# Kernel optimization log

Hardware: AMD Instinct MI355X
Metric: run time of the kernel (lower is better)

## Reference

```python
import jax, jax.numpy as jnp
from jax import lax
import numpy as np

FEAT_STRIDE = 16
PRE_NMS_TOP_N = 2000
POST_NMS_TOP_N = 300
NMS_THRESH = 0.7


def _whctrs(a):
    w = a[2] - a[0] + 1.0
    h = a[3] - a[1] + 1.0
    return w, h, a[0] + 0.5 * (w - 1.0), a[1] + 0.5 * (h - 1.0)


def _mkanchors(ws, hs, x_ctr, y_ctr):
    ws = np.asarray(ws, dtype=np.float64)
    hs = np.asarray(hs, dtype=np.float64)
    return np.stack([x_ctr - 0.5 * (ws - 1.0), y_ctr - 0.5 * (hs - 1.0),
                     x_ctr + 0.5 * (ws - 1.0), y_ctr + 0.5 * (hs - 1.0)], axis=1)


def generate_anchors(base_size=16, ratios=np.array([0.5, 1.0, 2.0]), scales=np.array([8.0, 16.0, 32.0])):
    base = np.array([1.0, 1.0, float(base_size), float(base_size)]) - 1.0
    w, h, xc, yc = _whctrs(base)
    size = w * h
    ws = np.round(np.sqrt(size / ratios))
    hs = np.round(ws * ratios)
    ratio_anchors = _mkanchors(ws, hs, xc, yc)
    out = []
    for i in range(ratio_anchors.shape[0]):
        w_i, h_i, xc_i, yc_i = _whctrs(ratio_anchors[i])
        out.append(_mkanchors(w_i * scales, h_i * scales, xc_i, yc_i))
    return np.vstack(out).astype(np.float32)


ANCHORS = generate_anchors()  # [A=9, 4]
NUM_ANCHORS = ANCHORS.shape[0]


def _nms_keep(boxes, thresh):
    # boxes [N,4], already sorted by descending score; torchvision IoU convention.
    x1, y1, x2, y2 = boxes[:, 0], boxes[:, 1], boxes[:, 2], boxes[:, 3]
    areas = (x2 - x1) * (y2 - y1)
    xx1 = jnp.maximum(x1[:, None], x1[None, :])
    yy1 = jnp.maximum(y1[:, None], y1[None, :])
    xx2 = jnp.minimum(x2[:, None], x2[None, :])
    yy2 = jnp.minimum(y2[:, None], y2[None, :])
    inter = jnp.clip(xx2 - xx1, 0.0) * jnp.clip(yy2 - yy1, 0.0)
    iou = inter / (areas[:, None] + areas[None, :] - inter + 1e-9)
    n = boxes.shape[0]
    # sup[i, j] True => box i (higher score) suppresses later box j
    sup = (iou > thresh) & jnp.triu(jnp.ones((n, n), bool), 1)

    def body(i, keep):
        return keep & ~(keep[i] & sup[i])

    return lax.fori_loop(0, n, body, jnp.ones((n,), bool))


def setup_inputs() -> dict:
    key = jax.random.key(0)
    k1, k2 = jax.random.split(key)
    B, A, H, W = 8, NUM_ANCHORS, 128, 128
    scores = jax.random.normal(k1, (B, 2 * A, H, W), jnp.float32)
    bbox_deltas = jax.random.normal(k2, (B, 4 * A, H, W), jnp.float32) * 0.2
    im_h = float(H * FEAT_STRIDE)
    im_w = float(W * FEAT_STRIDE)
    im_info = jnp.tile(jnp.array([[im_h, im_w, 1.0]], jnp.float32), (B, 1))
    return {"scores": scores, "bbox_deltas": bbox_deltas, "im_info": im_info}


def reference(scores, bbox_deltas, im_info):
    B, _, H, W = scores.shape
    A = NUM_ANCHORS
    # --- anchor generation over the feature grid ---
    sx = jnp.arange(W, dtype=jnp.float32) * FEAT_STRIDE
    sy = jnp.arange(H, dtype=jnp.float32) * FEAT_STRIDE
    gx, gy = jnp.meshgrid(sx, sy)  # 'xy' indexing matches np.meshgrid default
    shifts = jnp.stack([gx.ravel(), gy.ravel(), gx.ravel(), gy.ravel()], axis=1)  # [K,4]
    anchors = (jnp.asarray(ANCHORS)[None, :, :] + shifts[:, None, :]).reshape(-1, 4)  # [K*A,4]

    obj_scores = scores[:, A:].transpose(0, 2, 3, 1).reshape(B, -1)   # [B, K*A]
    deltas = bbox_deltas.transpose(0, 2, 3, 1).reshape(B, -1, 4)      # [B, K*A, 4]

    # --- bbox_transform_inv ---
    widths = anchors[:, 2] - anchors[:, 0] + 1.0
    heights = anchors[:, 3] - anchors[:, 1] + 1.0
    ctr_x = anchors[:, 0] + 0.5 * widths
    ctr_y = anchors[:, 1] + 0.5 * heights
    dx, dy, dw, dh = deltas[..., 0], deltas[..., 1], deltas[..., 2], deltas[..., 3]
    pred_ctr_x = dx * widths + ctr_x
    pred_ctr_y = dy * heights + ctr_y
    pred_w = jnp.exp(dw) * widths
    pred_h = jnp.exp(dh) * heights
    proposals = jnp.stack([pred_ctr_x - 0.5 * pred_w, pred_ctr_y - 0.5 * pred_h,
                           pred_ctr_x + 0.5 * pred_w, pred_ctr_y + 0.5 * pred_h], axis=-1)

    # --- clip_boxes: im_info[b] = (h, w, scale) ---
    max_x = (im_info[:, 1] - 1.0)[:, None]
    max_y = (im_info[:, 0] - 1.0)[:, None]
    proposals = jnp.stack([
        jnp.clip(proposals[..., 0], 0.0, max_x),
        jnp.clip(proposals[..., 1], 0.0, max_y),
        jnp.clip(proposals[..., 2], 0.0, max_x),
        jnp.clip(proposals[..., 3], 0.0, max_y)], axis=-1)

    # --- pre-NMS top-k by score ---
    _, order = lax.top_k(obj_scores, PRE_NMS_TOP_N)                  # [B, pre]
    top_props = jnp.take_along_axis(proposals, order[..., None], axis=1)  # [B, pre, 4]

    # --- per-image greedy NMS (fixed-size, jit-compatible) ---
    keep = jax.vmap(lambda b: _nms_keep(b, NMS_THRESH))(top_props)   # [B, pre] bool
    sel = jnp.argsort(jnp.where(keep, 0, 1), axis=1, stable=True)[:, :POST_NMS_TOP_N]
    valid = jnp.take_along_axis(keep, sel, axis=1)                   # [B, post]
    out_boxes = jnp.take_along_axis(top_props, sel[..., None], axis=1) * valid[..., None].astype(top_props.dtype)

    batch_idx = jnp.broadcast_to(
        jnp.arange(B, dtype=out_boxes.dtype)[:, None, None], (B, POST_NMS_TOP_N, 1))
    return jnp.concatenate([batch_idx, out_boxes], axis=-1)  # [B, post_nms_topN, 5]
```

## Files before the change

kernel.cpp:

```cpp
#include <hip/hip_runtime.h>

#define NB 8
#define NA 9
#define HH 128
#define WW 128
#define NCELL (HH * WW)
#define NTOT (NCELL * NA)
#define PRE_K 2000
#define POST_K 300
#define CAP 4096
#define HBLK 9
#define NMS_TH 0.7f

__constant__ float c_aw[NA] = {184.f, 368.f, 736.f, 128.f, 256.f, 512.f, 88.f, 176.f, 352.f};
__constant__ float c_ah[NA] = {96.f, 192.f, 384.f, 128.f, 256.f, 512.f, 176.f, 352.f, 704.f};

__device__ __forceinline__ unsigned int sortable(float s) {
    unsigned int u = __float_as_uint(s);
    return (u & 0x80000000u) ? ~u : (u | 0x80000000u);
}

__device__ __forceinline__ unsigned long long shflx64(unsigned long long v, int m) {
    return __shfl_xor(v, m, 64);
}

__global__ __launch_bounds__(1024) void hist0_kernel(const float* __restrict__ scores,
                                                     unsigned int* __restrict__ h0out) {
    __shared__ unsigned int h[2048];
    int b = blockIdx.y, tid = threadIdx.x;
    h[tid] = 0; h[tid + 1024] = 0;
    __syncthreads();
    const float4* sp4 = (const float4*)(scores + (size_t)b * 18 * NCELL + (size_t)NA * NCELL);
    int base4 = blockIdx.x * 4096;
#pragma unroll
    for (int e = 0; e < 4; ++e) {
        float4 v = sp4[base4 + e * 1024 + tid];
        atomicAdd(&h[sortable(v.x) >> 21], 1u);
        atomicAdd(&h[sortable(v.y) >> 21], 1u);
        atomicAdd(&h[sortable(v.z) >> 21], 1u);
        atomicAdd(&h[sortable(v.w) >> 21], 1u);
    }
    __syncthreads();
    unsigned int* o = h0out + ((size_t)(b * HBLK + blockIdx.x)) * 2048;
    o[tid] = h[tid];
    o[tid + 1024] = h[tid + 1024];
}

__global__ __launch_bounds__(1024) void select0_kernel(const unsigned int* __restrict__ h0out,
                                                       uint2* __restrict__ state0,
                                                       unsigned int* __restrict__ gh1,
                                                       int* __restrict__ cnt) {
    __shared__ unsigned int thr[1024];
    int b = blockIdx.x, tid = threadIdx.x;
    if (tid < 128) gh1[b * 128 + tid] = 0;
    if (tid == 0) cnt[b] = 0;
    unsigned int c0 = 0, c1 = 0;
    for (int p = 0; p < HBLK; ++p) {
        const unsigned int* hp = h0out + ((size_t)(b * HBLK + p)) * 2048;
        uint2 v = *(const uint2*)&hp[2 * tid];
        c0 += v.x; c1 += v.y;
    }
    thr[tid] = c0 + c1;
    __syncthreads();
    for (int off = 1; off < 1024; off <<= 1) {
        unsigned int v = (tid + off < 1024) ? thr[tid + off] : 0u;
        __syncthreads();
        thr[tid] += v;
        __syncthreads();
    }
    unsigned int above = (tid < 1023) ? thr[tid + 1] : 0u;
    if (thr[tid] >= (unsigned)PRE_K && above < (unsigned)PRE_K) {
        if (above + c1 >= (unsigned)PRE_K)
            state0[b] = make_uint2((unsigned)(2 * tid + 1), (unsigned)(PRE_K)-above);
        else
            state0[b] = make_uint2((unsigned)(2 * tid), (unsigned)(PRE_K)-above - c1);
    }
}

__global__ __launch_bounds__(1024) void hist1_kernel(const float* __restrict__ scores,
                                                     const uint2* __restrict__ state0,
                                                     unsigned int* __restrict__ gh1) {
    __shared__ unsigned int h[128];
    int b = blockIdx.y, tid = threadIdx.x;
    if (tid < 128) h[tid] = 0;
    __syncthreads();
    unsigned int piv = state0[b].x;
    const float4* sp4 = (const float4*)(scores + (size_t)b * 18 * NCELL + (size_t)NA * NCELL);
    int base4 = blockIdx.x * 4096;
#pragma unroll
    for (int e = 0; e < 4; ++e) {
        float4 v = sp4[base4 + e * 1024 + tid];
        unsigned int u;
        u = sortable(v.x); if ((u >> 21) == piv) atomicAdd(&h[(u >> 14) & 127u], 1u);
        u = sortable(v.y); if ((u >> 21) == piv) atomicAdd(&h[(u >> 14) & 127u], 1u);
        u = sortable(v.z); if ((u >> 21) == piv) atomicAdd(&h[(u >> 14) & 127u], 1u);
        u = sortable(v.w); if ((u >> 21) == piv) atomicAdd(&h[(u >> 14) & 127u], 1u);
    }
    __syncthreads();
    if (tid < 128 && h[tid]) atomicAdd(&gh1[b * 128 + tid], h[tid]);
}

__global__ void select1_kernel(const unsigned int* __restrict__ gh1,
                               const uint2* __restrict__ state0,
                               unsigned int* __restrict__ state1) {
    int b = blockIdx.x, lane = threadIdx.x;
    unsigned int c0 = 0, c1 = 0;
    if (lane < 64) {
        c0 = gh1[b * 128 + 2 * lane];
        c1 = gh1[b * 128 + 2 * lane + 1];
    }
    unsigned int sum = c0 + c1;
#pragma unroll
    for (int off = 1; off < 64; off <<= 1) {
        unsigned int v = __shfl_down(sum, off, 64);
        if (lane + off < 64) sum += v;
    }
    unsigned int above = __shfl_down(sum, 1, 64);
    if (lane == 63) above = 0;
    unsigned int need0 = state0[b].y;
    if (sum >= need0 && above < need0) {
        unsigned int d = (above + c1 >= need0) ? (unsigned)(2 * lane + 1) : (unsigned)(2 * lane);
        unsigned int prefix = (state0[b].x << 7) | d;
        state1[b] = prefix << 14;
    }
}

__global__ void gather_kernel(const float* __restrict__ scores,
                              const unsigned int* __restrict__ state1,
                              int* __restrict__ cnt,
                              unsigned long long* __restrict__ buf) {
    __shared__ unsigned long long lbuf[2048];
    __shared__ int lcnt;
    __shared__ int gbase;
    int b = blockIdx.y;
    int tid = threadIdx.x;
    if (tid == 0) lcnt = 0;
    __syncthreads();
    unsigned int P = state1[b];
    const float4* sp4 = (const float4*)(scores + (size_t)b * 18 * NCELL + (size_t)NA * NCELL);
    int base4 = blockIdx.x * 512;
#pragma unroll
    for (int e = 0; e < 2; ++e) {
        int t4 = base4 + e * 256 + tid;
        float4 v = sp4[t4];
        float el[4] = {v.x, v.y, v.z, v.w};
#pragma unroll
        for (int j = 0; j < 4; ++j) {
            unsigned int u = sortable(el[j]);
            if (u >= P) {
                int idx4 = t4 * 4 + j;
                int a = idx4 >> 14;
                int cell = idx4 & 16383;
                unsigned int i = (unsigned int)cell * 9u + (unsigned int)a;
                int pos = atomicAdd(&lcnt, 1);
                lbuf[pos] = ((unsigned long long)u << 32) |
                            (unsigned long long)(0xFFFFFFFFu - i);
            }
        }
    }
    __syncthreads();
    if (tid == 0) gbase = atomicAdd(&cnt[b], lcnt);
    __syncthreads();
    int m = lcnt, gb = gbase;
    for (int t = tid; t < m; t += 256) {
        int g = gb + t;
        if (g < CAP) buf[(size_t)b * CAP + g] = lbuf[t];
    }
}

#define SHFL_STEP(J)                                                          \
    {                                                                         \
        int d_ = (J) >> 1;                                                    \
        bool keepMax = (((tid & d_) == 0) == (((2u * (unsigned)tid) & k) == 0)); \
        unsigned long long pa = shflx64(va, d_);                              \
        unsigned long long pb = shflx64(vb, d_);                              \
        va = keepMax ? (va > pa ? va : pa) : (va < pa ? va : pa);             \
        vb = keepMax ? (vb > pb ? vb : pb) : (vb < pb ? vb : pb);             \
    }
#define LOCAL_STEP()                                                          \
    {                                                                         \
        bool desc = (((2u * (unsigned)tid) & k) == 0);                        \
        unsigned long long lo = va < vb ? va : vb;                            \
        unsigned long long hi = va < vb ? vb : va;                            \
        va = desc ? hi : lo; vb = desc ? lo : hi;                             \
    }

__global__ __launch_bounds__(1024) void sort_kernel(const unsigned long long* __restrict__ buf,
                                                    const int* __restrict__ cnt,
                                                    unsigned int* __restrict__ topidx) {
    __shared__ unsigned long long s[CAP];
    int b = blockIdx.x;
    int tid = threadIdx.x;
    int n = min(cnt[b], CAP);
    const unsigned long long* src = buf + (size_t)b * CAP;
    if (n <= 2048) {
        unsigned long long va = (2 * tid < n) ? src[2 * tid] : 0ULL;
        unsigned long long vb = (2 * tid + 1 < n) ? src[2 * tid + 1] : 0ULL;
#pragma unroll
        for (unsigned k = 2; k <= 128; k <<= 1) {
#pragma unroll
            for (unsigned j = k >> 1; j >= 2; j >>= 1) SHFL_STEP(j)
            LOCAL_STEP()
        }
        for (unsigned k = 256; k <= 2048; k <<= 1) {
            s[2 * tid] = va; s[2 * tid + 1] = vb;
            __syncthreads();
            for (unsigned j = k >> 1; j >= 128; j >>= 1) {
                for (int t = tid; t < 2048; t += 1024) {
                    int ixj = t ^ (int)j;
                    if (ixj > t) {
                        unsigned long long x = s[t], y = s[ixj];
                        if ((((unsigned)t & k) == 0) ? (x < y) : (x > y)) { s[t] = y; s[ixj] = x; }
                    }
                }
                __syncthreads();
            }
            va = s[2 * tid]; vb = s[2 * tid + 1];
#pragma unroll
            for (unsigned j = 64; j >= 2; j >>= 1) SHFL_STEP(j)
            LOCAL_STEP()
        }
        s[2 * tid] = va; s[2 * tid + 1] = vb;
        __syncthreads();
    } else {
        for (int t = tid; t < CAP; t += 1024)
            s[t] = (t < n) ? src[t] : 0ULL;
        __syncthreads();
        for (int k = 2; k <= CAP; k <<= 1) {
            for (int j = k >> 1; j > 0; j >>= 1) {
                for (int t = tid; t < CAP; t += 1024) {
                    int ixj = t ^ j;
                    if (ixj > t) {
                        unsigned long long x = s[t], y = s[ixj];
                        if (((t & k) == 0) ? (x < y) : (x > y)) { s[t] = y; s[ixj] = x; }
                    }
                }
                __syncthreads();
            }
        }
    }
    for (int r = tid; r < PRE_K; r += 1024)
        topidx[(size_t)b * PRE_K + r] = 0xFFFFFFFFu - (unsigned int)(s[r] & 0xFFFFFFFFu);
}

__global__ void decode_kernel(const unsigned int* __restrict__ topidx,
                              const float* __restrict__ deltas,
                              const float* __restrict__ im_info,
                              float4* __restrict__ props) {
    int gid = blockIdx.x * 256 + threadIdx.x;
    if (gid >= NB * PRE_K) return;
    int b = gid / PRE_K;
    unsigned int i = topidx[gid];
    unsigned int cell = i / 9u;
    unsigned int a = i - cell * 9u;
    int wx = (int)(cell & 127u), hy = (int)(cell >> 7);
    const float* dp = deltas + (size_t)b * 36 * NCELL + (size_t)(4u * a) * NCELL +
                      (size_t)hy * WW + wx;
    float dx = dp[0];
    float dy = dp[NCELL];
    float dw = dp[2 * NCELL];
    float dh = dp[3 * NCELL];
    float W_ = c_aw[a], H_ = c_ah[a];
    float cx = (float)(16 * wx + 8), cy = (float)(16 * hy + 8);
    float px = __fadd_rn(__fmul_rn(dx, W_), cx);
    float py = __fadd_rn(__fmul_rn(dy, H_), cy);
    float pw = __fmul_rn((float)exp((double)dw), W_);
    float ph = __fmul_rn((float)exp((double)dh), H_);
    float hw = __fmul_rn(0.5f, pw), hh = __fmul_rn(0.5f, ph);
    float x1 = __fsub_rn(px, hw), y1 = __fsub_rn(py, hh);
    float x2 = __fadd_rn(px, hw), y2 = __fadd_rn(py, hh);
    float maxx = __fsub_rn(im_info[b * 3 + 1], 1.0f);
    float maxy = __fsub_rn(im_info[b * 3 + 0], 1.0f);
    x1 = fminf(fmaxf(x1, 0.0f), maxx);
    y1 = fminf(fmaxf(y1, 0.0f), maxy);
    x2 = fminf(fmaxf(x2, 0.0f), maxx);
    y2 = fminf(fmaxf(y2, 0.0f), maxy);
    props[gid] = make_float4(x1, y1, x2, y2);
}

__global__ void mask_kernel(const float4* __restrict__ boxes,
                            unsigned long long* __restrict__ colm) {
    int iT = blockIdx.x, jT = blockIdx.y, b = blockIdx.z;
    if (iT > jT) return;
    __shared__ float4 ib[64];
    int t = threadIdx.x;
    int i0 = iT * 64;
    ib[t] = (i0 + t < PRE_K) ? boxes[(size_t)b * PRE_K + i0 + t] : make_float4(0.f, 0.f, -1.f, -1.f);
    __syncthreads();
    int j = jT * 64 + t;
    if (j >= PRE_K) return;
    float4 jb = boxes[(size_t)b * PRE_K + j];
    float barea = __fmul_rn(__fsub_rn(jb.z, jb.x), __fsub_rn(jb.w, jb.y));
    unsigned long long m = 0ULL;
    for (int ii = 0; ii < 64; ++ii) {
        int i = i0 + ii;
        if (i < j) {
            float4 c = ib[ii];
            float aarea = __fmul_rn(__fsub_rn(c.z, c.x), __fsub_rn(c.w, c.y));
            float xx1 = fmaxf(c.x, jb.x), yy1 = fmaxf(c.y, jb.y);
            float xx2 = fminf(c.z, jb.z), yy2 = fminf(c.w, jb.w);
            float iw = fmaxf(__fsub_rn(xx2, xx1), 0.0f);
            float ih = fmaxf(__fsub_rn(yy2, yy1), 0.0f);
            float inter = __fmul_rn(iw, ih);
            float denom = __fadd_rn(__fsub_rn(__fadd_rn(aarea, barea), inter), 1e-9f);
            float iou = __fdiv_rn(inter, denom);
            if (iou > NMS_TH) m |= (1ULL << ii);
        }
    }
    colm[((size_t)b * 32 + iT) * 2048 + j] = m;
}

__global__ void scan_kernel(const unsigned long long* __restrict__ colm,
                            const float4* __restrict__ boxes,
                            float* __restrict__ out) {
    int b = blockIdx.x;
    int lane = threadIdx.x;
    __shared__ unsigned long long kw[32];
    __shared__ int keeplist[POST_K];
    const unsigned long long* cb = colm + (size_t)b * 32 * 2048;
    int total = 0;
    bool done = false;
    for (int k = 0; k < 32 && !done; ++k) {
        int j = k * 64 + lane;
        unsigned long long d = 0;
        int w = 0;
        for (; w + 4 <= k; w += 4) {
            unsigned long long a0 = cb[(size_t)(w + 0) * 2048 + j] & kw[w + 0];
            unsigned long long a1 = cb[(size_t)(w + 1) * 2048 + j] & kw[w + 1];
            unsigned long long a2 = cb[(size_t)(w + 2) * 2048 + j] & kw[w + 2];
            unsigned long long a3 = cb[(size_t)(w + 3) * 2048 + j] & kw[w + 3];
            d |= (a0 | a1) | (a2 | a3);
        }
        for (; w < k; ++w) d |= cb[(size_t)w * 2048 + j] & kw[w];
        unsigned long long diag = cb[(size_t)k * 2048 + j];
        bool alive_me = (d == 0ULL) && (j < PRE_K);
        unsigned long long alive = __ballot(alive_me);
        unsigned long long keptw = 0ULL;
        while (alive) {
            int i = __builtin_ctzll(alive);
            keptw |= (1ULL << i);
            if (lane == 0) keeplist[total] = k * 64 + i;
            total++;
            if (total >= POST_K) { done = true; break; }
            unsigned long long sup = __ballot(((diag >> i) & 1ULL) != 0ULL);
            alive &= ~sup;
            alive &= ~keptw;
        }
        if (lane == 0) kw[k] = keptw;
        __syncthreads();
    }
    __syncthreads();
    int K = min(total, POST_K);
    const float4* bb = boxes + (size_t)b * PRE_K;
    for (int r = lane; r < POST_K; r += 64) {
        float4 v = make_float4(0.f, 0.f, 0.f, 0.f);
        if (r < K) v = bb[keeplist[r]];
        float* o = out + ((size_t)b * POST_K + r) * 5;
        o[0] = (float)b;
        o[1] = v.x;
        o[2] = v.y;
        o[3] = v.z;
        o[4] = v.w;
    }
}

extern "C" void kernel_launch(void* const* d_in, const int* in_sizes, int n_in,
                              void* d_out, int out_size, void* d_ws, size_t ws_size,
                              hipStream_t stream) {
    const float* scores = (const float*)d_in[0];
    const float* deltas = (const float*)d_in[1];
    const float* im_info = (const float*)d_in[2];
    float* out = (float*)d_out;
    char* ws = (char*)d_ws;

    unsigned int* h0out = (unsigned int*)(ws + 0);
    unsigned int* gh1 = (unsigned int*)(ws + 589824);
    uint2* state0 = (uint2*)(ws + 593920);
    unsigned int* state1 = (unsigned int*)(ws + 593984);
    int* cnt = (int*)(ws + 594048);
    unsigned long long* buf = (unsigned long long*)(ws + 594112);
    unsigned int* topidx = (unsigned int*)(ws + 856256);
    float4* props = (float4*)(ws + 920256);
    unsigned long long* colm = (unsigned long long*)(ws + 1176320);

    hipLaunchKernelGGL(hist0_kernel, dim3(HBLK, NB), dim3(1024), 0, stream, scores, h0out);
    hipLaunchKernelGGL(select0_kernel, dim3(NB), dim3(1024), 0, stream, h0out, state0, gh1, cnt);
    hipLaunchKernelGGL(hist1_kernel, dim3(HBLK, NB), dim3(1024), 0, stream, scores, state0, gh1);
    hipLaunchKernelGGL(select1_kernel, dim3(NB), dim3(64), 0, stream, gh1, state0, state1);
    hipLaunchKernelGGL(gather_kernel, dim3(72, NB), dim3(256), 0, stream, scores, state1, cnt, buf);
    hipLaunchKernelGGL(sort_kernel, dim3(NB), dim3(1024), 0, stream, buf, cnt, topidx);
    hipLaunchKernelGGL(decode_kernel, dim3((NB * PRE_K + 255) / 256), dim3(256), 0, stream,
                       topidx, deltas, im_info, props);
    hipLaunchKernelGGL(mask_kernel, dim3(32, 32, NB), dim3(64), 0, stream, props, colm);
    hipLaunchKernelGGL(scan_kernel, dim3(NB), dim3(64), 0, stream, colm, props, out);
}
```

Baseline: 106.1 us.

## Fuse all proposal pipeline stages into one cooperative kernel with grid syncs

```diff
diff --git a/kernel.cpp b/kernel.cpp
--- a/kernel.cpp
+++ b/kernel.cpp
@@ -1,4 +1,7 @@
 #include <hip/hip_runtime.h>
+#include <hip/hip_cooperative_groups.h>
+
+namespace cg = cooperative_groups;
 
 #define NB 8
 #define NA 9
@@ -9,7 +12,9 @@
 #define PRE_K 2000
 #define POST_K 300
 #define CAP 4096
-#define HBLK 9
+#define PARTS 18
+#define BLKS (NB * PARTS)
+#define TPB 1024
 #define NMS_TH 0.7f
 
 __constant__ float c_aw[NA] = {184.f, 368.f, 736.f, 128.f, 256.f, 512.f, 88.f, 176.f, 352.f};
@@ -22,150 +27,6 @@
 
 __device__ __forceinline__ unsigned long long shflx64(unsigned long long v, int m) {
     return __shfl_xor(v, m, 64);
-}
-
-__global__ __launch_bounds__(1024) void hist0_kernel(const float* __restrict__ scores,
-                                                     unsigned int* __restrict__ h0out) {
-    __shared__ unsigned int h[2048];
-    int b = blockIdx.y, tid = threadIdx.x;
-    h[tid] = 0; h[tid + 1024] = 0;
-    __syncthreads();
-    const float4* sp4 = (const float4*)(scores + (size_t)b * 18 * NCELL + (size_t)NA * NCELL);
-    int base4 = blockIdx.x * 4096;
-#pragma unroll
-    for (int e = 0; e < 4; ++e) {
-        float4 v = sp4[base4 + e * 1024 + tid];
-        atomicAdd(&h[sortable(v.x) >> 21], 1u);
-        atomicAdd(&h[sortable(v.y) >> 21], 1u);
-        atomicAdd(&h[sortable(v.z) >> 21], 1u);
-        atomicAdd(&h[sortable(v.w) >> 21], 1u);
-    }
-    __syncthreads();
-    unsigned int* o = h0out + ((size_t)(b * HBLK + blockIdx.x)) * 2048;
-    o[tid] = h[tid];
-    o[tid + 1024] = h[tid + 1024];
-}
-
-__global__ __launch_bounds__(1024) void select0_kernel(const unsigned int* __restrict__ h0out,
-                                                       uint2* __restrict__ state0,
-                                                       unsigned int* __restrict__ gh1,
-                                                       int* __restrict__ cnt) {
-    __shared__ unsigned int thr[1024];
-    int b = blockIdx.x, tid = threadIdx.x;
-    if (tid < 128) gh1[b * 128 + tid] = 0;
-    if (tid == 0) cnt[b] = 0;
-    unsigned int c0 = 0, c1 = 0;
-    for (int p = 0; p < HBLK; ++p) {
-        const unsigned int* hp = h0out + ((size_t)(b * HBLK + p)) * 2048;
-        uint2 v = *(const uint2*)&hp[2 * tid];
-        c0 += v.x; c1 += v.y;
-    }
-    thr[tid] = c0 + c1;
-    __syncthreads();
-    for (int off = 1; off < 1024; off <<= 1) {
-        unsigned int v = (tid + off < 1024) ? thr[tid + off] : 0u;
-        __syncthreads();
-        thr[tid] += v;
-        __syncthreads();
-    }
-    unsigned int above = (tid < 1023) ? thr[tid + 1] : 0u;
-    if (thr[tid] >= (unsigned)PRE_K && above < (unsigned)PRE_K) {
-        if (above + c1 >= (unsigned)PRE_K)
-            state0[b] = make_uint2((unsigned)(2 * tid + 1), (unsigned)(PRE_K)-above);
-        else
-            state0[b] = make_uint2((unsigned)(2 * tid), (unsigned)(PRE_K)-above - c1);
-    }
-}
-
-__global__ __launch_bounds__(1024) void hist1_kernel(const float* __restrict__ scores,
-                                                     const uint2* __restrict__ state0,
-                                                     unsigned int* __restrict__ gh1) {
-    __shared__ unsigned int h[128];
-    int b = blockIdx.y, tid = threadIdx.x;
-    if (tid < 128) h[tid] = 0;
-    __syncthreads();
-    unsigned int piv = state0[b].x;
-    const float4* sp4 = (const float4*)(scores + (size_t)b * 18 * NCELL + (size_t)NA * NCELL);
-    int base4 = blockIdx.x * 4096;
-#pragma unroll
-    for (int e = 0; e < 4; ++e) {
-        float4 v = sp4[base4 + e * 1024 + tid];
-        unsigned int u;
-        u = sortable(v.x); if ((u >> 21) == piv) atomicAdd(&h[(u >> 14) & 127u], 1u);
-        u = sortable(v.y); if ((u >> 21) == piv) atomicAdd(&h[(u >> 14) & 127u], 1u);
-        u = sortable(v.z); if ((u >> 21) == piv) atomicAdd(&h[(u >> 14) & 127u], 1u);
-        u = sortable(v.w); if ((u >> 21) == piv) atomicAdd(&h[(u >> 14) & 127u], 1u);
-    }
-    __syncthreads();
-    if (tid < 128 && h[tid]) atomicAdd(&gh1[b * 128 + tid], h[tid]);
-}
-
-__global__ void select1_kernel(const unsigned int* __restrict__ gh1,
-                               const uint2* __restrict__ state0,
-                               unsigned int* __restrict__ state1) {
-    int b = blockIdx.x, lane = threadIdx.x;
-    unsigned int c0 = 0, c1 = 0;
-    if (lane < 64) {
-        c0 = gh1[b * 128 + 2 * lane];
-        c1 = gh1[b * 128 + 2 * lane + 1];
-    }
-    unsigned int sum = c0 + c1;
-#pragma unroll
-    for (int off = 1; off < 64; off <<= 1) {
-        unsigned int v = __shfl_down(sum, off, 64);
-        if (lane + off < 64) sum += v;
-    }
-    unsigned int above = __shfl_down(sum, 1, 64);
-    if (lane == 63) above = 0;
-    unsigned int need0 = state0[b].y;
-    if (sum >= need0 && above < need0) {
-        unsigned int d = (above + c1 >= need0) ? (unsigned)(2 * lane + 1) : (unsigned)(2 * lane);
-        unsigned int prefix = (state0[b].x << 7) | d;
-        state1[b] = prefix << 14;
-    }
-}
-
-__global__ void gather_kernel(const float* __restrict__ scores,
-                              const unsigned int* __restrict__ state1,
-                              int* __restrict__ cnt,
-                              unsigned long long* __restrict__ buf) {
-    __shared__ unsigned long long lbuf[2048];
-    __shared__ int lcnt;
-    __shared__ int gbase;
-    int b = blockIdx.y;
-    int tid = threadIdx.x;
-    if (tid == 0) lcnt = 0;
-    __syncthreads();
-    unsigned int P = state1[b];
-    const float4* sp4 = (const float4*)(scores + (size_t)b * 18 * NCELL + (size_t)NA * NCELL);
-    int base4 = blockIdx.x * 512;
-#pragma unroll
-    for (int e = 0; e < 2; ++e) {
-        int t4 = base4 + e * 256 + tid;
-        float4 v = sp4[t4];
-        float el[4] = {v.x, v.y, v.z, v.w};
-#pragma unroll
-        for (int j = 0; j < 4; ++j) {
-            unsigned int u = sortable(el[j]);
-            if (u >= P) {
-                int idx4 = t4 * 4 + j;
-                int a = idx4 >> 14;
-                int cell = idx4 & 16383;
-                unsigned int i = (unsigned int)cell * 9u + (unsigned int)a;
-                int pos = atomicAdd(&lcnt, 1);
-                lbuf[pos] = ((unsigned long long)u << 32) |
-                            (unsigned long long)(0xFFFFFFFFu - i);
-            }
-        }
-    }
-    __syncthreads();
-    if (tid == 0) gbase = atomicAdd(&cnt[b], lcnt);
-    __syncthreads();
-    int m = lcnt, gb = gbase;
-    for (int t = tid; t < m; t += 256) {
-        int g = gb + t;
-        if (g < CAP) buf[(size_t)b * CAP + g] = lbuf[t];
-    }
 }
 
 #define SHFL_STEP(J)                                                          \
@@ -185,182 +46,319 @@
         va = desc ? hi : lo; vb = desc ? lo : hi;                             \
     }
 
-__global__ __launch_bounds__(1024) void sort_kernel(const unsigned long long* __restrict__ buf,
-                                                    const int* __restrict__ cnt,
-                                                    unsigned int* __restrict__ topidx) {
-    __shared__ unsigned long long s[CAP];
-    int b = blockIdx.x;
-    int tid = threadIdx.x;
-    int n = min(cnt[b], CAP);
-    const unsigned long long* src = buf + (size_t)b * CAP;
-    if (n <= 2048) {
-        unsigned long long va = (2 * tid < n) ? src[2 * tid] : 0ULL;
-        unsigned long long vb = (2 * tid + 1 < n) ? src[2 * tid + 1] : 0ULL;
+__global__ __launch_bounds__(TPB) void fused_kernel(
+    const float* __restrict__ scores, const float* __restrict__ deltas,
+    const float* __restrict__ im_info,
+    unsigned int* __restrict__ h0out, unsigned int* __restrict__ gh1,
+    uint2* __restrict__ state0, unsigned int* __restrict__ state1,
+    int* __restrict__ cnt, unsigned long long* __restrict__ buf,
+    unsigned int* __restrict__ topidx, float4* __restrict__ props,
+    unsigned long long* __restrict__ colm, float* __restrict__ out) {
+    cg::grid_group grid = cg::this_grid();
+    __shared__ __align__(16) unsigned char smem[33024];
+    const int BID = blockIdx.x;
+    const int tid = threadIdx.x;
+    const int b = BID / PARTS;
+    const int part = BID % PARTS;
+
+    const float4* sp4 = (const float4*)(scores + (size_t)b * 18 * NCELL + (size_t)NA * NCELL);
+    const int base4 = part * 2048;
+    float4 v0 = sp4[base4 + tid];
+    float4 v1 = sp4[base4 + 1024 + tid];
+    unsigned int u0 = sortable(v0.x), u1 = sortable(v0.y), u2 = sortable(v0.z), u3 = sortable(v0.w);
+    unsigned int u4 = sortable(v1.x), u5 = sortable(v1.y), u6 = sortable(v1.z), u7 = sortable(v1.w);
+    {
+        unsigned int* h2 = (unsigned int*)smem;
+        h2[tid] = 0; h2[tid + 1024] = 0;
+        __syncthreads();
+        atomicAdd(&h2[u0 >> 21], 1u); atomicAdd(&h2[u1 >> 21], 1u);
+        atomicAdd(&h2[u2 >> 21], 1u); atomicAdd(&h2[u3 >> 21], 1u);
+        atomicAdd(&h2[u4 >> 21], 1u); atomicAdd(&h2[u5 >> 21], 1u);
+        atomicAdd(&h2[u6 >> 21], 1u); atomicAdd(&h2[u7 >> 21], 1u);
+        __syncthreads();
+        h0out[(size_t)BID * 2048 + tid] = h2[tid];
+        h0out[(size_t)BID * 2048 + tid + 1024] = h2[tid + 1024];
+    }
+    grid.sync();
+
+    if (BID < NB) {
+        const int sb = BID;
+        unsigned int* thr = (unsigned int*)smem;
+        if (tid < 128) gh1[sb * 128 + tid] = 0;
+        if (tid == 0) cnt[sb] = 0;
+        unsigned int c0 = 0, c1 = 0;
+        for (int p = 0; p < PARTS; ++p) {
+            const unsigned int* hp = h0out + (size_t)(sb * PARTS + p) * 2048;
+            uint2 v = *(const uint2*)&hp[2 * tid];
+            c0 += v.x; c1 += v.y;
+        }
+        thr[tid] = c0 + c1;
+        __syncthreads();
+        for (int off = 1; off < 1024; off <<= 1) {
+            unsigned int v = (tid + off < 1024) ? thr[tid + off] : 0u;
+            __syncthreads();
+            thr[tid] += v;
+            __syncthreads();
+        }
+        unsigned int above = (tid < 1023) ? thr[tid + 1] : 0u;
+        if (thr[tid] >= (unsigned)PRE_K && above < (unsigned)PRE_K) {
+            if (above + c1 >= (unsigned)PRE_K)
+                state0[sb] = make_uint2((unsigned)(2 * tid + 1), (unsigned)(PRE_K)-above);
+            else
+                state0[sb] = make_uint2((unsigned)(2 * tid), (unsigned)(PRE_K)-above - c1);
+        }
+    }
+    grid.sync();
+
+    {
+        unsigned int* h128 = (unsigned int*)smem;
+        if (tid < 128) h128[tid] = 0;
+        __syncthreads();
+        unsigned int piv = state0[b].x;
+#define TEST(U) if (((U) >> 21) == piv) atomicAdd(&h128[((U) >> 14) & 127u], 1u);
+        TEST(u0) TEST(u1) TEST(u2) TEST(u3) TEST(u4) TEST(u5) TEST(u6) TEST(u7)
+#undef TEST
+        __syncthreads();
+        if (tid < 128 && h128[tid]) atomicAdd(&gh1[b * 128 + tid], h128[tid]);
+    }
+    grid.sync();
+
+    if (BID < NB && tid < 64) {
+        const int sb = BID, lane = tid;
+        unsigned int c0 = gh1[sb * 128 + 2 * lane];
+        unsigned int c1 = gh1[sb * 128 + 2 * lane + 1];
+        unsigned int sum = c0 + c1;
 #pragma unroll
-        for (unsigned k = 2; k <= 128; k <<= 1) {
+        for (int off = 1; off < 64; off <<= 1) {
+            unsigned int v = __shfl_down(sum, off, 64);
+            if (lane + off < 64) sum += v;
+        }
+        unsigned int above = __shfl_down(sum, 1, 64);
+        if (lane == 63) above = 0;
+        unsigned int need0 = state0[sb].y;
+        if (sum >= need0 && above < need0) {
+            unsigned int d = (above + c1 >= need0) ? (unsigned)(2 * lane + 1) : (unsigned)(2 * lane);
+            state1[sb] = ((state0[sb].x << 7) | d) << 14;
+        }
+    }
+    grid.sync();
+
+    {
+        unsigned long long* lbuf = (unsigned long long*)smem;
+        int* lmisc = (int*)(smem + 16384);
+        if (tid == 0) lmisc[0] = 0;
+        __syncthreads();
+        unsigned int P = state1[b];
+        int e0 = (base4 + tid) * 4;
+        int e1 = (base4 + 1024 + tid) * 4;
+#define GATH(U, IDX4)                                                         \
+        if ((U) >= P) {                                                       \
+            int a_ = (IDX4) >> 14;                                            \
+            int cell_ = (IDX4) & 16383;                                       \
+            unsigned int i_ = (unsigned int)cell_ * 9u + (unsigned int)a_;    \
+            int pos_ = atomicAdd(&lmisc[0], 1);                               \
+            if (pos_ < 2048)                                                  \
+                lbuf[pos_] = ((unsigned long long)(U) << 32) |                \
+                             (unsigned long long)(0xFFFFFFFFu - i_);          \
+        }
+        GATH(u0, e0) GATH(u1, e0 + 1) GATH(u2, e0 + 2) GATH(u3, e0 + 3)
+        GATH(u4, e1) GATH(u5, e1 + 1) GATH(u6, e1 + 2) GATH(u7, e1 + 3)
+#undef GATH
+        __syncthreads();
+        if (tid == 0) lmisc[1] = atomicAdd(&cnt[b], lmisc[0]);
+        __syncthreads();
+        int m = min(lmisc[0], 2048), gb = lmisc[1];
+        for (int t = tid; t < m; t += TPB) {
+            int g = gb + t;
+            if (g < CAP) buf[(size_t)b * CAP + g] = lbuf[t];
+        }
+    }
+    grid.sync();
+
+    if (BID < NB) {
+        unsigned long long* s = (unsigned long long*)smem;
+        int n = min(cnt[BID], CAP);
+        const unsigned long long* src = buf + (size_t)BID * CAP;
+        if (n <= 2048) {
+            unsigned long long va = (2 * tid < n) ? src[2 * tid] : 0ULL;
+            unsigned long long vb = (2 * tid + 1 < n) ? src[2 * tid + 1] : 0ULL;
 #pragma unroll
-            for (unsigned j = k >> 1; j >= 2; j >>= 1) SHFL_STEP(j)
-            LOCAL_STEP()
-        }
-        for (unsigned k = 256; k <= 2048; k <<= 1) {
+            for (unsigned k = 2; k <= 128; k <<= 1) {
+#pragma unroll
+                for (unsigned j = k >> 1; j >= 2; j >>= 1) SHFL_STEP(j)
+                LOCAL_STEP()
+            }
+            for (unsigned k = 256; k <= 2048; k <<= 1) {
+                s[2 * tid] = va; s[2 * tid + 1] = vb;
+                __syncthreads();
+                for (unsigned j = k >> 1; j >= 128; j >>= 1) {
+                    for (int t = tid; t < 2048; t += TPB) {
+                        int ixj = t ^ (int)j;
+                        if (ixj > t) {
+                            unsigned long long x = s[t], y = s[ixj];
+                            if ((((unsigned)t & k) == 0) ? (x < y) : (x > y)) { s[t] = y; s[ixj] = x; }
+                        }
+                    }
+                    __syncthreads();
+                }
+                va = s[2 * tid]; vb = s[2 * tid + 1];
+#pragma unroll
+                for (unsigned j = 64; j >= 2; j >>= 1) SHFL_STEP(j)
+                LOCAL_STEP()
+            }
             s[2 * tid] = va; s[2 * tid + 1] = vb;
             __syncthreads();
-            for (unsigned j = k >> 1; j >= 128; j >>= 1) {
-                for (int t = tid; t < 2048; t += 1024) {
-                    int ixj = t ^ (int)j;
-                    if (ixj > t) {
-                        unsigned long long x = s[t], y = s[ixj];
-                        if ((((unsigned)t & k) == 0) ? (x < y) : (x > y)) { s[t] = y; s[ixj] = x; }
+        } else {
+            for (int t = tid; t < CAP; t += TPB)
+                s[t] = (t < n) ? src[t] : 0ULL;
+            __syncthreads();
+            for (int k = 2; k <= CAP; k <<= 1) {
+                for (int j = k >> 1; j > 0; j >>= 1) {
+                    for (int t = tid; t < CAP; t += TPB) {
+                        int ixj = t ^ j;
+                        if (ixj > t) {
+                            unsigned long long x = s[t], y = s[ixj];
+                            if (((t & k) == 0) ? (x < y) : (x > y)) { s[t] = y; s[ixj] = x; }
+                        }
                     }
-                }
-                __syncthreads();
-            }
-            va = s[2 * tid]; vb = s[2 * tid + 1];
-#pragma unroll
-            for (unsigned j = 64; j >= 2; j >>= 1) SHFL_STEP(j)
-            LOCAL_STEP()
-        }
-        s[2 * tid] = va; s[2 * tid + 1] = vb;
-        __syncthreads();
-    } else {
-        for (int t = tid; t < CAP; t += 1024)
-            s[t] = (t < n) ? src[t] : 0ULL;
-        __syncthreads();
-        for (int k = 2; k <= CAP; k <<= 1) {
-            for (int j = k >> 1; j > 0; j >>= 1) {
-                for (int t = tid; t < CAP; t += 1024) {
-                    int ixj = t ^ j;
-                    if (ixj > t) {
-                        unsigned long long x = s[t], y = s[ixj];
-                        if (((t & k) == 0) ? (x < y) : (x > y)) { s[t] = y; s[ixj] = x; }
+                    __syncthreads();
+                }
+            }
+        }
+        for (int r = tid; r < PRE_K; r += TPB)
+            topidx[(size_t)BID * PRE_K + r] = 0xFFFFFFFFu - (unsigned int)(s[r] & 0xFFFFFFFFu);
+    }
+    grid.sync();
+
+    {
+        int gid = BID * TPB + tid;
+        if (gid < NB * PRE_K) {
+            int db = gid / PRE_K;
+            unsigned int i = topidx[gid];
+            unsigned int cell = i / 9u;
+            unsigned int a = i - cell * 9u;
+            int wx = (int)(cell & 127u), hy = (int)(cell >> 7);
+            const float* dp = deltas + (size_t)db * 36 * NCELL + (size_t)(4u * a) * NCELL +
+                              (size_t)hy * WW + wx;
+            float dx = dp[0];
+            float dy = dp[NCELL];
+            float dw = dp[2 * NCELL];
+            float dh = dp[3 * NCELL];
+            float W_ = c_aw[a], H_ = c_ah[a];
+            float cx = (float)(16 * wx + 8), cy = (float)(16 * hy + 8);
+            float px = __fadd_rn(__fmul_rn(dx, W_), cx);
+            float py = __fadd_rn(__fmul_rn(dy, H_), cy);
+            float pw = __fmul_rn((float)exp((double)dw), W_);
+            float ph = __fmul_rn((float)exp((double)dh), H_);
+            float hw = __fmul_rn(0.5f, pw), hh = __fmul_rn(0.5f, ph);
+            float x1 = __fsub_rn(px, hw), y1 = __fsub_rn(py, hh);
+            float x2 = __fadd_rn(px, hw), y2 = __fadd_rn(py, hh);
+            float maxx = __fsub_rn(im_info[db * 3 + 1], 1.0f);
+            float maxy = __fsub_rn(im_info[db * 3 + 0], 1.0f);
+            x1 = fminf(fmaxf(x1, 0.0f), maxx);
+            y1 = fminf(fmaxf(y1, 0.0f), maxy);
+            x2 = fminf(fmaxf(x2, 0.0f), maxx);
+            y2 = fminf(fmaxf(y2, 0.0f), maxy);
+            props[gid] = make_float4(x1, y1, x2, y2);
+        }
+    }
+    grid.sync();
+
+    {
+        float4* sbox = (float4*)smem;
+        for (int p = BID; p < NB * 32; p += BLKS) {
+            int pb = p >> 5, jT = p & 31;
+            __syncthreads();
+            for (int t = tid; t < PRE_K; t += TPB) sbox[t] = props[pb * PRE_K + t];
+            __syncthreads();
+            int jl = tid & 63, g = tid >> 6;
+            int j = jT * 64 + jl;
+            float4 jb = sbox[j];
+            float barea = __fmul_rn(__fsub_rn(jb.z, jb.x), __fsub_rn(jb.w, jb.y));
+            for (int iT = g; iT <= jT; iT += 16) {
+                unsigned long long m = 0ULL;
+                int i0 = iT * 64;
+#pragma unroll 8
+                for (int ii = 0; ii < 64; ++ii) {
+                    int i = i0 + ii;
+                    if (i < j) {
+                        float4 c = sbox[i0 + ii];
+                        float aarea = __fmul_rn(__fsub_rn(c.z, c.x), __fsub_rn(c.w, c.y));
+                        float xx1 = fmaxf(c.x, jb.x), yy1 = fmaxf(c.y, jb.y);
+                        float xx2 = fminf(c.z, jb.z), yy2 = fminf(c.w, jb.w);
+                        float iw = fmaxf(__fsub_rn(xx2, xx1), 0.0f);
+                        float ih = fmaxf(__fsub_rn(yy2, yy1), 0.0f);
+                        float inter = __fmul_rn(iw, ih);
+                        float denom = __fadd_rn(__fsub_rn(__fadd_rn(aarea, barea), inter), 1e-9f);
+                        float iou = __fdiv_rn(inter, denom);
+                        if (iou > NMS_TH) m |= (1ULL << ii);
                     }
                 }
-                __syncthreads();
-            }
-        }
-    }
-    for (int r = tid; r < PRE_K; r += 1024)
-        topidx[(size_t)b * PRE_K + r] = 0xFFFFFFFFu - (unsigned int)(s[r] & 0xFFFFFFFFu);
-}
-
-__global__ void decode_kernel(const unsigned int* __restrict__ topidx,
-                              const float* __restrict__ deltas,
-                              const float* __restrict__ im_info,
-                              float4* __restrict__ props) {
-    int gid = blockIdx.x * 256 + threadIdx.x;
-    if (gid >= NB * PRE_K) return;
-    int b = gid / PRE_K;
-    unsigned int i = topidx[gid];
-    unsigned int cell = i / 9u;
-    unsigned int a = i - cell * 9u;
-    int wx = (int)(cell & 127u), hy = (int)(cell >> 7);
-    const float* dp = deltas + (size_t)b * 36 * NCELL + (size_t)(4u * a) * NCELL +
-                      (size_t)hy * WW + wx;
-    float dx = dp[0];
-    float dy = dp[NCELL];
-    float dw = dp[2 * NCELL];
-    float dh = dp[3 * NCELL];
-    float W_ = c_aw[a], H_ = c_ah[a];
-    float cx = (float)(16 * wx + 8), cy = (float)(16 * hy + 8);
-    float px = __fadd_rn(__fmul_rn(dx, W_), cx);
-    float py = __fadd_rn(__fmul_rn(dy, H_), cy);
-    float pw = __fmul_rn((float)exp((double)dw), W_);
-    float ph = __fmul_rn((float)exp((double)dh), H_);
-    float hw = __fmul_rn(0.5f, pw), hh = __fmul_rn(0.5f, ph);
-    float x1 = __fsub_rn(px, hw), y1 = __fsub_rn(py, hh);
-    float x2 = __fadd_rn(px, hw), y2 = __fadd_rn(py, hh);
-    float maxx = __fsub_rn(im_info[b * 3 + 1], 1.0f);
-    float maxy = __fsub_rn(im_info[b * 3 + 0], 1.0f);
-    x1 = fminf(fmaxf(x1, 0.0f), maxx);
-    y1 = fminf(fmaxf(y1, 0.0f), maxy);
-    x2 = fminf(fmaxf(x2, 0.0f), maxx);
-    y2 = fminf(fmaxf(y2, 0.0f), maxy);
-    props[gid] = make_float4(x1, y1, x2, y2);
-}
-
-__global__ void mask_kernel(const float4* __restrict__ boxes,
-                            unsigned long long* __restrict__ colm) {
-    int iT = blockIdx.x, jT = blockIdx.y, b = blockIdx.z;
-    if (iT > jT) return;
-    __shared__ float4 ib[64];
-    int t = threadIdx.x;
-    int i0 = iT * 64;
-    ib[t] = (i0 + t < PRE_K) ? boxes[(size_t)b * PRE_K + i0 + t] : make_float4(0.f, 0.f, -1.f, -1.f);
-    __syncthreads();
-    int j = jT * 64 + t;
-    if (j >= PRE_K) return;
-    float4 jb = boxes[(size_t)b * PRE_K + j];
-    float barea = __fmul_rn(__fsub_rn(jb.z, jb.x), __fsub_rn(jb.w, jb.y));
-    unsigned long long m = 0ULL;
-    for (int ii = 0; ii < 64; ++ii) {
-        int i = i0 + ii;
-        if (i < j) {
-            float4 c = ib[ii];
-            float aarea = __fmul_rn(__fsub_rn(c.z, c.x), __fsub_rn(c.w, c.y));
-            float xx1 = fmaxf(c.x, jb.x), yy1 = fmaxf(c.y, jb.y);
-            float xx2 = fminf(c.z, jb.z), yy2 = fminf(c.w, jb.w);
-            float iw = fmaxf(__fsub_rn(xx2, xx1), 0.0f);
-            float ih = fmaxf(__fsub_rn(yy2, yy1), 0.0f);
-            float inter = __fmul_rn(iw, ih);
-            float denom = __fadd_rn(__fsub_rn(__fadd_rn(aarea, barea), inter), 1e-9f);
-            float iou = __fdiv_rn(inter, denom);
-            if (iou > NMS_TH) m |= (1ULL << ii);
-        }
-    }
-    colm[((size_t)b * 32 + iT) * 2048 + j] = m;
-}
-
-__global__ void scan_kernel(const unsigned long long* __restrict__ colm,
-                            const float4* __restrict__ boxes,
-                            float* __restrict__ out) {
-    int b = blockIdx.x;
-    int lane = threadIdx.x;
-    __shared__ unsigned long long kw[32];
-    __shared__ int keeplist[POST_K];
-    const unsigned long long* cb = colm + (size_t)b * 32 * 2048;
-    int total = 0;
-    bool done = false;
-    for (int k = 0; k < 32 && !done; ++k) {
-        int j = k * 64 + lane;
-        unsigned long long d = 0;
-        int w = 0;
-        for (; w + 4 <= k; w += 4) {
-            unsigned long long a0 = cb[(size_t)(w + 0) * 2048 + j] & kw[w + 0];
-            unsigned long long a1 = cb[(size_t)(w + 1) * 2048 + j] & kw[w + 1];
-            unsigned long long a2 = cb[(size_t)(w + 2) * 2048 + j] & kw[w + 2];
-            unsigned long long a3 = cb[(size_t)(w + 3) * 2048 + j] & kw[w + 3];
-            d |= (a0 | a1) | (a2 | a3);
-        }
-        for (; w < k; ++w) d |= cb[(size_t)w * 2048 + j] & kw[w];
-        unsigned long long diag = cb[(size_t)k * 2048 + j];
-        bool alive_me = (d == 0ULL) && (j < PRE_K);
-        unsigned long long alive = __ballot(alive_me);
-        unsigned long long keptw = 0ULL;
-        while (alive) {
-            int i = __builtin_ctzll(alive);
-            keptw |= (1ULL << i);
-            if (lane == 0) keeplist[total] = k * 64 + i;
-            total++;
-            if (total >= POST_K) { done = true; break; }
-            unsigned long long sup = __ballot(((diag >> i) & 1ULL) != 0ULL);
-            alive &= ~sup;
-            alive &= ~keptw;
-        }
-        if (lane == 0) kw[k] = keptw;
-        __syncthreads();
-    }
-    __syncthreads();
-    int K = min(total, POST_K);
-    const float4* bb = boxes + (size_t)b * PRE_K;
-    for (int r = lane; r < POST_K; r += 64) {
-        float4 v = make_float4(0.f, 0.f, 0.f, 0.f);
-        if (r < K) v = bb[keeplist[r]];
-        float* o = out + ((size_t)b * POST_K + r) * 5;
-        o[0] = (float)b;
-        o[1] = v.x;
-        o[2] = v.y;
-        o[3] = v.z;
-        o[4] = v.w;
+                colm[((size_t)pb * 32 + iT) * 2048 + j] = m;
+            }
+        }
+    }
+    grid.sync();
+
+    if (BID >= NB) return;
+    {
+        unsigned long long* kw = (unsigned long long*)smem;
+        int* keeplist = (int*)(smem + 256);
+        int* sctl = (int*)(smem + 256 + POST_K * 4);
+        if (tid == 0) { sctl[0] = 0; sctl[1] = 0; }
+        __syncthreads();
+        const unsigned long long* cb = colm + (size_t)BID * 32 * 2048;
+        int total = 0;
+        for (int k = 0; k < 32; ++k) {
+            if (tid < 64) {
+                int lane = tid;
+                int j = k * 64 + lane;
+                unsigned long long d = 0;
+                int w = 0;
+                for (; w + 4 <= k; w += 4) {
+                    unsigned long long a0 = cb[(size_t)(w + 0) * 2048 + j] & kw[w + 0];
+                    unsigned long long a1 = cb[(size_t)(w + 1) * 2048 + j] & kw[w + 1];
+                    unsigned long long a2 = cb[(size_t)(w + 2) * 2048 + j] & kw[w + 2];
+                    unsigned long long a3 = cb[(size_t)(w + 3) * 2048 + j] & kw[w + 3];
+                    d |= (a0 | a1) | (a2 | a3);
+                }
+                for (; w < k; ++w) d |= cb[(size_t)w * 2048 + j] & kw[w];
+                unsigned long long diag = cb[(size_t)k * 2048 + j];
+                bool alive_me = (d == 0ULL) && (j < PRE_K);
+                unsigned long long alive = __ballot(alive_me);
+                unsigned long long keptw = 0ULL;
+                while (alive) {
+                    int i = __builtin_ctzll(alive);
+                    keptw |= (1ULL << i);
+                    if (lane == 0 && total < POST_K) keeplist[total] = k * 64 + i;
+                    total++;
+                    if (total >= POST_K) break;
+                    unsigned long long sup = __ballot(((diag >> i) & 1ULL) != 0ULL);
+                    alive &= ~sup;
+                    alive &= ~keptw;
+                }
+                if (lane == 0) {
+                    kw[k] = keptw;
+                    sctl[0] = (total >= POST_K) ? 1 : 0;
+                    sctl[1] = total;
+                }
+            }
+            __syncthreads();
+            if (sctl[0]) break;
+        }
+        __syncthreads();
+        int K = min(sctl[1], POST_K);
+        const float4* bb = props + (size_t)BID * PRE_K;
+        for (int r = tid; r < POST_K; r += TPB) {
+            float4 v = make_float4(0.f, 0.f, 0.f, 0.f);
+            if (r < K) v = bb[keeplist[r]];
+            float* o = out + ((size_t)BID * POST_K + r) * 5;
+            o[0] = (float)BID;
+            o[1] = v.x;
+            o[2] = v.y;
+            o[3] = v.z;
+            o[4] = v.w;
+        }
     }
 }
 
@@ -374,23 +372,19 @@
     char* ws = (char*)d_ws;
 
     unsigned int* h0out = (unsigned int*)(ws + 0);
-    unsigned int* gh1 = (unsigned int*)(ws + 589824);
-    uint2* state0 = (uint2*)(ws + 593920);
-    unsigned int* state1 = (unsigned int*)(ws + 593984);
-    int* cnt = (int*)(ws + 594048);
-    unsigned long long* buf = (unsigned long long*)(ws + 594112);
-    unsigned int* topidx = (unsigned int*)(ws + 856256);
-    float4* props = (float4*)(ws + 920256);
-    unsigned long long* colm = (unsigned long long*)(ws + 1176320);
-
-    hipLaunchKernelGGL(hist0_kernel, dim3(HBLK, NB), dim3(1024), 0, stream, scores, h0out);
-    hipLaunchKernelGGL(select0_kernel, dim3(NB), dim3(1024), 0, stream, h0out, state0, gh1, cnt);
-    hipLaunchKernelGGL(hist1_kernel, dim3(HBLK, NB), dim3(1024), 0, stream, scores, state0, gh1);
-    hipLaunchKernelGGL(select1_kernel, dim3(NB), dim3(64), 0, stream, gh1, state0, state1);
-    hipLaunchKernelGGL(gather_kernel, dim3(72, NB), dim3(256), 0, stream, scores, state1, cnt, buf);
-    hipLaunchKernelGGL(sort_kernel, dim3(NB), dim3(1024), 0, stream, buf, cnt, topidx);
-    hipLaunchKernelGGL(decode_kernel, dim3((NB * PRE_K + 255) / 256), dim3(256), 0, stream,
-                       topidx, deltas, im_info, props);
-    hipLaunchKernelGGL(mask_kernel, dim3(32, 32, NB), dim3(64), 0, stream, props, colm);
-    hipLaunchKernelGGL(scan_kernel, dim3(NB), dim3(64), 0, stream, colm, props, out);
+    unsigned int* gh1 = (unsigned int*)(ws + 1179648);
+    uint2* state0 = (uint2*)(ws + 1183744);
+    unsigned int* state1 = (unsigned int*)(ws + 1183808);
+    int* cnt = (int*)(ws + 1183872);
+    unsigned long long* buf = (unsigned long long*)(ws + 1183936);
+    unsigned int* topidx = (unsigned int*)(ws + 1446080);
+    float4* props = (float4*)(ws + 1510080);
+    unsigned long long* colm = (unsigned long long*)(ws + 1766080);
+
+    void* args[] = {(void*)&scores, (void*)&deltas, (void*)&im_info,
+                    (void*)&h0out, (void*)&gh1, (void*)&state0, (void*)&state1,
+                    (void*)&cnt, (void*)&buf, (void*)&topidx, (void*)&props,
+                    (void*)&colm, (void*)&out};
+    hipLaunchCooperativeKernel((void*)fused_kernel, dim3(BLKS), dim3(TPB),
+                               args, 0, stream);
 }
```

After: 237.9 us. +124.3%, slower.
